# Optimization experiments

Measured on AMD Instinct MI355X. Metric: run time of the kernel, lower is better.

The kernel has to match this reference:

```python
import jax, jax.numpy as jnp
import numpy as np
from jax import lax


def setup_inputs() -> dict:
    key = jax.random.key(0)
    k1, k2, k3, k4 = jax.random.split(key, 4)
    B, C, H, W = 4, 1024, 64, 64
    OUT = 2048
    refer_feat = jax.random.normal(k1, (B, C, H, W), jnp.float32)
    sup_feat = jax.random.normal(k2, (B, C, H, W), jnp.float32)
    # al_conv_one: Conv2d(2048 -> 2, k=3, pad=1); small init keeps offsets in a sane range
    w_off = jax.random.normal(k3, (2, 2 * C, 3, 3), jnp.float32) * 0.01
    b_off = jnp.zeros((2,), jnp.float32)
    # defConv1: DeformConv2d(1024 -> 2048, k=1, bias=False); weight is effectively [O, C]
    w_def = jax.random.normal(k4, (OUT, C), jnp.float32) * (1.0 / np.sqrt(C))
    return {"refer_feat": refer_feat, "sup_feat": sup_feat,
            "w_off": w_off, "b_off": b_off, "w_def": w_def}


def _deform_sample(feat, dy, dx):
    """Bilinear-sample feat[b,:, h+dy, w+dx] with zero padding outside. -> [B,C,H*W]"""
    B, C, H, W = feat.shape
    py = dy + jnp.arange(H, dtype=feat.dtype)[None, :, None]   # [B,H,W]
    px = dx + jnp.arange(W, dtype=feat.dtype)[None, None, :]   # [B,H,W]
    y0 = jnp.floor(py)
    x0 = jnp.floor(px)
    wy1 = py - y0   # frac weights
    wx1 = px - x0
    y0i = y0.astype(jnp.int32)
    x0i = x0.astype(jnp.int32)
    feat_flat = feat.reshape(B, C, H * W)

    def corner(yi, xi, wgt):
        valid = (yi >= 0) & (yi < H) & (xi >= 0) & (xi < W)
        idx = (jnp.clip(yi, 0, H - 1) * W + jnp.clip(xi, 0, W - 1)).reshape(B, 1, H * W)
        g = jnp.take_along_axis(feat_flat, idx, axis=2)          # [B,C,HW]
        return g * (wgt * valid.astype(feat.dtype)).reshape(B, 1, H * W)

    return (corner(y0i, x0i, (1 - wy1) * (1 - wx1))
            + corner(y0i, x0i + 1, (1 - wy1) * wx1)
            + corner(y0i + 1, x0i, wy1 * (1 - wx1))
            + corner(y0i + 1, x0i + 1, wy1 * wx1))


def reference(refer_feat, sup_feat, w_off, b_off, w_def):
    B, C, H, W = sup_feat.shape
    concat_feat = jnp.concatenate([refer_feat, sup_feat], axis=1)      # [B,2C,H,W]
    offset = lax.conv_general_dilated(
        concat_feat, w_off, window_strides=(1, 1), padding='SAME',
        dimension_numbers=('NCHW', 'OIHW', 'NCHW')) + b_off[None, :, None, None]  # [B,2,H,W]
    # torchvision DeformConv2d offset layout for k=1: channel 0 = dy, channel 1 = dx
    sampled = _deform_sample(sup_feat, offset[:, 0], offset[:, 1])     # [B,C,HW]
    out = jnp.einsum('oc,bcl->bol', w_def, sampled)                    # 1x1 conv as GEMM
    return out.reshape(B, w_def.shape[0], H, W)
```

## Files before the change

### kernel.cpp

```cpp
#include <hip/hip_runtime.h>

#define CC   1024
#define C2   2048
#define HH   64
#define WW   64
#define HW   4096
#define MOUT 2048
#define NB   4
#define LP   40

typedef short  short8  __attribute__((ext_vector_type(8)));
typedef float  floatx4 __attribute__((ext_vector_type(4)));

static __device__ __forceinline__ unsigned short f2bf(float f) {
  unsigned int u = __builtin_bit_cast(unsigned int, f);
  u = u + 0x7FFFu + ((u >> 16) & 1u);
  return (unsigned short)(u >> 16);
}

__global__ __launch_bounds__(256)
void conv_off(const float* __restrict__ refer, const float* __restrict__ sup,
              const float* __restrict__ woff, float* __restrict__ off)
{
  const int cz = blockIdx.x;
  const int ry = blockIdx.y;
  const int b  = blockIdx.z;
  const int wv = threadIdx.x >> 6;
  const int w  = threadIdx.x & 63;
  const int h0 = ry * 8 + wv * 2;

  float a00 = 0.f, a01 = 0.f, a10 = 0.f, a11 = 0.f;
  const int cbase = cz * 64;

  for (int ci = 0; ci < 64; ci++) {
    const int cc = cbase + ci;
    const float* plane = (cc < CC) ? (refer + ((size_t)b * CC + cc) * HW)
                                   : (sup   + ((size_t)b * CC + (cc - CC)) * HW);
    float r[4];
#pragma unroll
    for (int j = 0; j < 4; j++) {
      const int gy = h0 - 1 + j;
      r[j] = (gy >= 0 && gy < HH) ? plane[gy * WW + w] : 0.f;
    }
    float lft[4], rgt[4];
#pragma unroll
    for (int j = 0; j < 4; j++) {
      const float tl = __shfl(r[j], (w - 1) & 63, 64);
      const float tr = __shfl(r[j], (w + 1) & 63, 64);
      lft[j] = (w == 0)  ? 0.f : tl;
      rgt[j] = (w == 63) ? 0.f : tr;
    }
    const float* wp0 = woff + (size_t)cc * 9;
    const float* wp1 = woff + (size_t)(C2 + cc) * 9;
#pragma unroll
    for (int ky = 0; ky < 3; ky++) {
      const float w00 = wp0[ky * 3 + 0], w01 = wp0[ky * 3 + 1], w02 = wp0[ky * 3 + 2];
      const float w10 = wp1[ky * 3 + 0], w11 = wp1[ky * 3 + 1], w12 = wp1[ky * 3 + 2];
      a00 += lft[ky]     * w00 + r[ky]     * w01 + rgt[ky]     * w02;
      a01 += lft[ky]     * w10 + r[ky]     * w11 + rgt[ky]     * w12;
      a10 += lft[ky + 1] * w00 + r[ky + 1] * w01 + rgt[ky + 1] * w02;
      a11 += lft[ky + 1] * w10 + r[ky + 1] * w11 + rgt[ky + 1] * w12;
    }
  }

  atomicAdd(&off[((b * 2 + 0) * HH + h0) * WW + w],     a00);
  atomicAdd(&off[((b * 2 + 1) * HH + h0) * WW + w],     a01);
  atomicAdd(&off[((b * 2 + 0) * HH + h0 + 1) * WW + w], a10);
  atomicAdd(&off[((b * 2 + 1) * HH + h0 + 1) * WW + w], a11);
}

__global__ __launch_bounds__(256)
void cvt_bf16(const float* __restrict__ src, unsigned short* __restrict__ dst, int n4)
{
  const int i = blockIdx.x * 256 + threadIdx.x;
  if (i < n4) {
    const float4 f = ((const float4*)src)[i];
    ushort4 u;
    u.x = f2bf(f.x); u.y = f2bf(f.y); u.z = f2bf(f.z); u.w = f2bf(f.w);
    ((ushort4*)dst)[i] = u;
  }
}

__global__ __launch_bounds__(256)
void sample_kern(const float* __restrict__ sup, const float* __restrict__ off,
                 const float* __restrict__ boff, unsigned short* __restrict__ St)
{
  const int h   = blockIdx.x;
  const int b   = blockIdx.y;
  const int tid = threadIdx.x;

  __shared__ float swy[64], swx[64];
  __shared__ int   sy0[64], sx0[64];
  __shared__ unsigned short tile[64 * 68];

  if (tid < 64) {
    const float dy = off[((b * 2 + 0) * HH + h) * WW + tid] + boff[0];
    const float dx = off[((b * 2 + 1) * HH + h) * WW + tid] + boff[1];
    const float py = dy + (float)h;
    const float px = dx + (float)tid;
    const float y0f = floorf(py), x0f = floorf(px);
    sy0[tid] = (int)y0f;  sx0[tid] = (int)x0f;
    swy[tid] = py - y0f;  swx[tid] = px - x0f;
  }
  __syncthreads();

  const int l   = tid & 63;
  const int cs0 = tid >> 6;
  const int y0 = sy0[l], x0 = sx0[l];
  const int y1 = y0 + 1, x1 = x0 + 1;
  const float wy1 = swy[l], wx1 = swx[l];
  const float wy0 = 1.f - wy1, wx0 = 1.f - wx1;
  const float vy0 = (y0 >= 0 && y0 < HH) ? 1.f : 0.f;
  const float vy1 = (y1 >= 0 && y1 < HH) ? 1.f : 0.f;
  const float vx0 = (x0 >= 0 && x0 < WW) ? 1.f : 0.f;
  const float vx1 = (x1 >= 0 && x1 < WW) ? 1.f : 0.f;
  const int cy0 = min(max(y0, 0), HH - 1), cy1 = min(max(y1, 0), HH - 1);
  const int cx0 = min(max(x0, 0), WW - 1), cx1 = min(max(x1, 0), WW - 1);
  const int i00 = cy0 * WW + cx0, i01 = cy0 * WW + cx1;
  const int i10 = cy1 * WW + cx0, i11 = cy1 * WW + cx1;
  const float w00 = wy0 * wx0 * vy0 * vx0;
  const float w01 = wy0 * wx1 * vy0 * vx1;
  const float w10 = wy1 * wx0 * vy1 * vx0;
  const float w11 = wy1 * wx1 * vy1 * vx1;

  const int cq  = tid & 15;
  const int ls0 = tid >> 4;
  unsigned short* stb = St + ((size_t)b * HW + h * 64) * CC;

  for (int ct = 0; ct < 16; ct++) {
    const int cb = ct * 64;
    for (int cs = cs0; cs < 64; cs += 4) {
      const float* sp = sup + ((size_t)b * CC + cb + cs) * HW;
      const float v = w00 * sp[i00] + w01 * sp[i01] + w10 * sp[i10] + w11 * sp[i11];
      tile[cs * 68 + l] = f2bf(v);
    }
    __syncthreads();
    for (int ls = ls0; ls < 64; ls += 16) {
      ushort4 pk;
      pk.x = tile[(cq * 4 + 0) * 68 + ls];
      pk.y = tile[(cq * 4 + 1) * 68 + ls];
      pk.z = tile[(cq * 4 + 2) * 68 + ls];
      pk.w = tile[(cq * 4 + 3) * 68 + ls];
      *(ushort4*)&stb[(size_t)ls * CC + cb + cq * 4] = pk;
    }
    __syncthreads();
  }
}

__global__ __launch_bounds__(256)
void gemm_bt(const unsigned short* __restrict__ A,
             const unsigned short* __restrict__ Bt,
             float* __restrict__ C)
{
  const int bb = blockIdx.z;
  const int n0 = blockIdx.x * 128;
  const int m0 = blockIdx.y * 128;
  const unsigned short* Bb = Bt + (size_t)bb * HW * CC;
  float* Cb = C + (size_t)bb * (size_t)MOUT * HW;

  __shared__ unsigned short lA[128 * LP];
  __shared__ unsigned short lB[128 * LP];

  const int tid  = threadIdx.x;
  const int wave = tid >> 6;
  const int lane = tid & 63;
  const int wm   = (wave >> 1) * 64;
  const int wn   = (wave & 1) * 64;
  const int lrow = lane & 15;
  const int quad = lane >> 4;

  const int srow = tid >> 1;
  const int scol = (tid & 1) * 16;

  floatx4 acc[4][4];
#pragma unroll
  for (int i = 0; i < 4; i++)
#pragma unroll
    for (int j = 0; j < 4; j++)
      acc[i][j] = (floatx4){0.f, 0.f, 0.f, 0.f};

  const unsigned short* ga = A  + (size_t)(m0 + srow) * CC + scol;
  const unsigned short* gb = Bb + (size_t)(n0 + srow) * CC + scol;
  unsigned short* la = &lA[srow * LP + scol];
  unsigned short* lb = &lB[srow * LP + scol];

  for (int k0 = 0; k0 < CC; k0 += 32) {
    const uint4 a0 = *(const uint4*)(ga + k0);
    const uint4 a1 = *(const uint4*)(ga + k0 + 8);
    const uint4 b0 = *(const uint4*)(gb + k0);
    const uint4 b1 = *(const uint4*)(gb + k0 + 8);
    __syncthreads();
    *(uint4*)la       = a0;
    *(uint4*)(la + 8) = a1;
    *(uint4*)lb       = b0;
    *(uint4*)(lb + 8) = b1;
    __syncthreads();

    short8 af[4], bfr[4];
#pragma unroll
    for (int t = 0; t < 4; t++) {
      af[t]  = *(const short8*)&lA[(wm + t * 16 + lrow) * LP + quad * 8];
      bfr[t] = *(const short8*)&lB[(wn + t * 16 + lrow) * LP + quad * 8];
    }
#pragma unroll
    for (int i = 0; i < 4; i++)
#pragma unroll
      for (int j = 0; j < 4; j++)
        acc[i][j] = __builtin_amdgcn_mfma_f32_16x16x32_bf16(af[i], bfr[j], acc[i][j], 0, 0, 0);
  }

#pragma unroll
  for (int i = 0; i < 4; i++) {
    const int mbase = m0 + wm + i * 16 + quad * 4;
#pragma unroll
    for (int j = 0; j < 4; j++) {
      const int n = n0 + wn + j * 16 + lrow;
      float* cp = Cb + (size_t)mbase * HW + n;
#pragma unroll
      for (int r = 0; r < 4; r++)
        cp[(size_t)r * HW] = acc[i][j][r];
    }
  }
}

extern "C" void kernel_launch(void* const* d_in, const int* in_sizes, int n_in,
                              void* d_out, int out_size, void* d_ws, size_t ws_size,
                              hipStream_t stream)
{
  const float* refer = (const float*)d_in[0];
  const float* sup   = (const float*)d_in[1];
  const float* woff  = (const float*)d_in[2];
  const float* boff  = (const float*)d_in[3];
  const float* wdef  = (const float*)d_in[4];
  float* out = (float*)d_out;

  char* ws = (char*)d_ws;
  float* off            = (float*)ws;
  unsigned short* wdefb = (unsigned short*)(ws + (512u << 10));
  unsigned short* St    = (unsigned short*)(ws + (512u << 10) + (4u << 20));

  hipMemsetAsync(off, 0, (size_t)NB * 2 * HW * sizeof(float), stream);
  conv_off<<<dim3(32, 8, NB), 256, 0, stream>>>(refer, sup, woff, off);
  cvt_bf16<<<dim3((MOUT * CC / 4 + 255) / 256), 256, 0, stream>>>(wdef, wdefb, MOUT * CC / 4);
  sample_kern<<<dim3(HH, NB), 256, 0, stream>>>(sup, off, boff, St);
  gemm_bt<<<dim3(HW / 128, MOUT / 128, NB), 256, 0, stream>>>(wdefb, St, out);
}
```

Measured before the change: 455.2 us.

## Use direct global-to-LDS loads with XOR swizzle in GEMM; parallelize sampling over channels

The GEMM now loads A and B tiles straight into LDS with global_load_lds 16-byte transfers, using a K=64 tile and an XOR-swizzled layout in place of register staging and a padded layout. This is meant to cut register round-trips and LDS bank conflicts, and to halve the number of barriers per K. The sampling kernel gains a grid dimension over 64-channel tiles, so it launches 16x more blocks in place of looping, which raises occupancy for the gather. The risk is that the 16-byte global_load_lds form depends on gfx950 support, and the swizzle indexing has to match exactly between the load side and the read side.

```diff
diff --git a/kernel.cpp b/kernel.cpp
--- a/kernel.cpp
+++ b/kernel.cpp
@@ -7,7 +7,6 @@
 #define HW   4096
 #define MOUT 2048
 #define NB   4
-#define LP   40
 
 typedef short  short8  __attribute__((ext_vector_type(8)));
 typedef float  floatx4 __attribute__((ext_vector_type(4)));
@@ -16,6 +15,12 @@
   unsigned int u = __builtin_bit_cast(unsigned int, f);
   u = u + 0x7FFFu + ((u >> 16) & 1u);
   return (unsigned short)(u >> 16);
+}
+
+static __device__ __forceinline__ void glds16(const unsigned short* g, unsigned short* l) {
+  __builtin_amdgcn_global_load_lds(
+      (const __attribute__((address_space(1))) void*)g,
+      (__attribute__((address_space(3))) void*)l, 16, 0, 0);
 }
 
 __global__ __launch_bounds__(256)
@@ -86,7 +91,8 @@
                  const float* __restrict__ boff, unsigned short* __restrict__ St)
 {
   const int h   = blockIdx.x;
-  const int b   = blockIdx.y;
+  const int ct  = blockIdx.y;
+  const int b   = blockIdx.z;
   const int tid = threadIdx.x;
 
   __shared__ float swy[64], swx[64];
@@ -123,27 +129,23 @@
   const float w10 = wy1 * wx0 * vy1 * vx0;
   const float w11 = wy1 * wx1 * vy1 * vx1;
 
+  const int cb = ct * 64;
+  for (int cs = cs0; cs < 64; cs += 4) {
+    const float* sp = sup + ((size_t)b * CC + cb + cs) * HW;
+    const float v = w00 * sp[i00] + w01 * sp[i01] + w10 * sp[i10] + w11 * sp[i11];
+    tile[cs * 68 + l] = f2bf(v);
+  }
+  __syncthreads();
   const int cq  = tid & 15;
   const int ls0 = tid >> 4;
   unsigned short* stb = St + ((size_t)b * HW + h * 64) * CC;
-
-  for (int ct = 0; ct < 16; ct++) {
-    const int cb = ct * 64;
-    for (int cs = cs0; cs < 64; cs += 4) {
-      const float* sp = sup + ((size_t)b * CC + cb + cs) * HW;
-      const float v = w00 * sp[i00] + w01 * sp[i01] + w10 * sp[i10] + w11 * sp[i11];
-      tile[cs * 68 + l] = f2bf(v);
-    }
-    __syncthreads();
-    for (int ls = ls0; ls < 64; ls += 16) {
-      ushort4 pk;
-      pk.x = tile[(cq * 4 + 0) * 68 + ls];
-      pk.y = tile[(cq * 4 + 1) * 68 + ls];
-      pk.z = tile[(cq * 4 + 2) * 68 + ls];
-      pk.w = tile[(cq * 4 + 3) * 68 + ls];
-      *(ushort4*)&stb[(size_t)ls * CC + cb + cq * 4] = pk;
-    }
-    __syncthreads();
+  for (int ls = ls0; ls < 64; ls += 16) {
+    ushort4 pk;
+    pk.x = tile[(cq * 4 + 0) * 68 + ls];
+    pk.y = tile[(cq * 4 + 1) * 68 + ls];
+    pk.z = tile[(cq * 4 + 2) * 68 + ls];
+    pk.w = tile[(cq * 4 + 3) * 68 + ls];
+    *(ushort4*)&stb[(size_t)ls * CC + cb + cq * 4] = pk;
   }
 }
 
@@ -158,8 +160,8 @@
   const unsigned short* Bb = Bt + (size_t)bb * HW * CC;
   float* Cb = C + (size_t)bb * (size_t)MOUT * HW;
 
-  __shared__ unsigned short lA[128 * LP];
-  __shared__ unsigned short lB[128 * LP];
+  __shared__ __align__(16) unsigned short lA[128 * 64];
+  __shared__ __align__(16) unsigned short lB[128 * 64];
 
   const int tid  = threadIdx.x;
   const int wave = tid >> 6;
@@ -169,8 +171,10 @@
   const int lrow = lane & 15;
   const int quad = lane >> 4;
 
-  const int srow = tid >> 1;
-  const int scol = (tid & 1) * 16;
+  const int g8 = lane >> 3;
+  const int s8 = (lane & 7) ^ g8;
+  const unsigned short* gA = A  + (size_t)(m0 + wave * 32 + g8) * CC + s8 * 8;
+  const unsigned short* gB = Bb + (size_t)(n0 + wave * 32 + g8) * CC + s8 * 8;
 
   floatx4 acc[4][4];
 #pragma unroll
@@ -179,34 +183,30 @@
     for (int j = 0; j < 4; j++)
       acc[i][j] = (floatx4){0.f, 0.f, 0.f, 0.f};
 
-  const unsigned short* ga = A  + (size_t)(m0 + srow) * CC + scol;
-  const unsigned short* gb = Bb + (size_t)(n0 + srow) * CC + scol;
-  unsigned short* la = &lA[srow * LP + scol];
-  unsigned short* lb = &lB[srow * LP + scol];
-
-  for (int k0 = 0; k0 < CC; k0 += 32) {
-    const uint4 a0 = *(const uint4*)(ga + k0);
-    const uint4 a1 = *(const uint4*)(ga + k0 + 8);
-    const uint4 b0 = *(const uint4*)(gb + k0);
-    const uint4 b1 = *(const uint4*)(gb + k0 + 8);
+  for (int k0 = 0; k0 < CC; k0 += 64) {
     __syncthreads();
-    *(uint4*)la       = a0;
-    *(uint4*)(la + 8) = a1;
-    *(uint4*)lb       = b0;
-    *(uint4*)(lb + 8) = b1;
+#pragma unroll
+    for (int q = 0; q < 4; q++) {
+      glds16(gA + (size_t)q * 8 * CC + k0, &lA[(wave * 32 + q * 8) * 64]);
+      glds16(gB + (size_t)q * 8 * CC + k0, &lB[(wave * 32 + q * 8) * 64]);
+    }
     __syncthreads();
 
-    short8 af[4], bfr[4];
-#pragma unroll
-    for (int t = 0; t < 4; t++) {
-      af[t]  = *(const short8*)&lA[(wm + t * 16 + lrow) * LP + quad * 8];
-      bfr[t] = *(const short8*)&lB[(wn + t * 16 + lrow) * LP + quad * 8];
-    }
-#pragma unroll
-    for (int i = 0; i < 4; i++)
-#pragma unroll
-      for (int j = 0; j < 4; j++)
-        acc[i][j] = __builtin_amdgcn_mfma_f32_16x16x32_bf16(af[i], bfr[j], acc[i][j], 0, 0, 0);
+#pragma unroll
+    for (int ks = 0; ks < 2; ks++) {
+      short8 af[4], bfr[4];
+#pragma unroll
+      for (int t = 0; t < 4; t++) {
+        const int sw = ((ks * 4 + quad) ^ (lrow & 7)) * 8;
+        af[t]  = *(const short8*)&lA[(wm + t * 16 + lrow) * 64 + sw];
+        bfr[t] = *(const short8*)&lB[(wn + t * 16 + lrow) * 64 + sw];
+      }
+#pragma unroll
+      for (int i = 0; i < 4; i++)
+#pragma unroll
+        for (int j = 0; j < 4; j++)
+          acc[i][j] = __builtin_amdgcn_mfma_f32_16x16x32_bf16(af[i], bfr[j], acc[i][j], 0, 0, 0);
+    }
   }
 
 #pragma unroll
@@ -242,6 +242,6 @@
   hipMemsetAsync(off, 0, (size_t)NB * 2 * HW * sizeof(float), stream);
   conv_off<<<dim3(32, 8, NB), 256, 0, stream>>>(refer, sup, woff, off);
   cvt_bf16<<<dim3((MOUT * CC / 4 + 255) / 256), 256, 0, stream>>>(wdef, wdefb, MOUT * CC / 4);
-  sample_kern<<<dim3(HH, NB), 256, 0, stream>>>(sup, off, boff, St);
+  sample_kern<<<dim3(HH, 16, NB), 256, 0, stream>>>(sup, off, boff, St);
   gemm_bt<<<dim3(HW / 128, MOUT / 128, NB), 256, 0, stream>>>(wdefb, St, out);
 }
```

Result: faster. 401.1 us (-11.9%).
